# Performance work log

Measured on AMD Instinct MI355X. Metric: run time of the kernel, lower is better.

Reference implementation:

```python
import jax, jax.numpy as jnp
import numpy as np

K = 512
D = 256


def setup_inputs() -> dict:
    key = jax.random.key(0)
    k1, k2 = jax.random.split(key)
    x = jax.random.normal(k1, (64, D, 32, 32), dtype=jnp.float32)
    # nn.Embedding(K, D) init: uniform(-1/K, 1/K)
    emb = jax.random.uniform(k2, (K, D), dtype=jnp.float32, minval=-1.0 / K, maxval=1.0 / K)
    return {"x": x, "emb": emb}


def reference(x, emb):
    # encoder is identity: z_e_x = x, shape [B, D, H, W]
    B, Dd, H, W = x.shape
    z_e = jnp.transpose(x, (0, 2, 3, 1))           # [B, H, W, D]
    z_flat = z_e.reshape(-1, Dd)                    # [N, D]
    # squared euclidean distances to codebook: ||z||^2 + ||e||^2 - 2 z.e
    dist = (jnp.sum(z_flat * z_flat, axis=1, keepdims=True)
            + jnp.sum(emb * emb, axis=1)[None, :]
            - 2.0 * z_flat @ emb.T)                 # [N, K]
    idx = jnp.argmin(dist, axis=1)                  # [N]
    codes = emb[idx]                                # [N, D] gather
    codes = codes.reshape(B, H, W, Dd)
    # straight-through quantized output (value == codes)
    z_q_st = z_e + jax.lax.stop_gradient(codes - z_e)
    z_q_st = jnp.transpose(z_q_st, (0, 3, 1, 2))    # [B, D, H, W]
    # z_q_x_bar: gathered from live codebook (grads flow to emb)
    z_q_bar = jnp.transpose(codes, (0, 3, 1, 2))    # [B, D, H, W]
    # decoder is identity: x_tilde = z_q_st
    return (z_q_st, x, z_q_bar)
```

## Files before the change

### kernel.cpp

```cpp
#include <hip/hip_runtime.h>


#define B_  64
#define D_  256
#define HW_ 1024
#define K_  512

typedef __attribute__((ext_vector_type(8))) short short8;
typedef __attribute__((ext_vector_type(4))) float f32x4;

__device__ unsigned short g_ebf[K_ * D_];
__device__ float g_e2[K_];

__device__ __forceinline__ unsigned short f2bf(float f) {
    unsigned u = __float_as_uint(f);
    u += 0x7fffu + ((u >> 16) & 1u);
    return (unsigned short)(u >> 16);
}

__global__ void prep(const float* __restrict__ emb) {
    const int t   = threadIdx.x;
    const int row = blockIdx.x * 8 + (t >> 5);
    const int c0  = (t & 31) * 8;
    const float* rp = emb + row * D_ + c0;
    float4 a = *(const float4*)rp;
    float4 b = *(const float4*)(rp + 4);
    short8 v;
    v[0] = (short)f2bf(a.x); v[1] = (short)f2bf(a.y);
    v[2] = (short)f2bf(a.z); v[3] = (short)f2bf(a.w);
    v[4] = (short)f2bf(b.x); v[5] = (short)f2bf(b.y);
    v[6] = (short)f2bf(b.z); v[7] = (short)f2bf(b.w);
    *(short8*)(g_ebf + row * D_ + c0) = v;
    float ps = a.x*a.x + a.y*a.y + a.z*a.z + a.w*a.w
             + b.x*b.x + b.y*b.y + b.z*b.z + b.w*b.w;
    ps += __shfl_xor(ps, 1);  ps += __shfl_xor(ps, 2);
    ps += __shfl_xor(ps, 4);  ps += __shfl_xor(ps, 8);
    ps += __shfl_xor(ps, 16);
    if ((t & 31) == 0) g_e2[row] = ps;
}

__global__ __launch_bounds__(128, 4)
void vq_main(const float* __restrict__ x, const float* __restrict__ emb,
             float* __restrict__ out0, float* __restrict__ out1,
             float* __restrict__ out2) {
    __shared__ float zc[4][32][32];
    __shared__ float mval[2][32];
    __shared__ int   midx[2][32];
    __shared__ int   fidx[32];

    const int t   = threadIdx.x;
    const int w   = t >> 6;
    const int l   = t & 63;
    const int blk = blockIdx.x;
    const int b   = blk >> 5;
    const int hw0 = (blk & 31) << 5;
    const float* xb = x    + ((size_t)b * D_) * HW_ + hw0;
    float*       o1 = out1 + ((size_t)b * D_) * HW_ + hw0;

    short8 zb[2][8];
    for (int r = 0; r < 2; ++r) {
#pragma unroll
        for (int gg = 0; gg < 2; ++gg) {
            const int g = 4 * r + 2 * w + gg;
#pragma unroll
            for (int it = 0; it < 4; ++it) {
                const float* gp = xb + (size_t)(32 * g + 8 * it + (l >> 3)) * HW_ + (l & 7) * 4;
                float* lp = &zc[g & 3][8 * it][0];
                __builtin_amdgcn_global_load_lds(
                    (const __attribute__((address_space(1))) unsigned int*)gp,
                    (__attribute__((address_space(3))) unsigned int*)lp,
                    16, 0, 0);
            }
        }
        __syncthreads();
#pragma unroll
        for (int g4 = 0; g4 < 4; ++g4) {
            const int g = 4 * r + g4;
#pragma unroll
            for (int t2 = 0; t2 < 2; ++t2) {
                const int p = 16 * t2 + (l & 15);
                short8 f;
#pragma unroll
                for (int j = 0; j < 8; ++j)
                    f[j] = (short)f2bf(zc[g4][(l >> 4) * 8 + j][p]);
                zb[t2][g] = f;
            }
        }
#pragma unroll
        for (int gg = 0; gg < 2; ++gg) {
            const int g = 4 * r + 2 * w + gg;
#pragma unroll
            for (int it = 0; it < 4; ++it) {
                const int dr = 32 * g + 8 * it + (l >> 3);
                float4 v = *(const float4*)&zc[g & 3][8 * it + (l >> 3)][(l & 7) * 4];
                *(float4*)&o1[(size_t)dr * HW_ + (l & 7) * 4] = v;
            }
        }
        __syncthreads();
    }

    float minv0 = 3.0e38f, minv1 = 3.0e38f;
    int   mini0 = 0,       mini1 = 0;
    short8 ea[8], eb[8];
    f32x4  e2a, e2b;
    const int ctbase = w * 16;

#define LOADE(buf, e2r, ct) do {                                              \
        const unsigned short* _p = g_ebf + ((ct) * 16 + (l & 15)) * D_        \
                                   + (l >> 4) * 8;                            \
        _Pragma("unroll")                                                     \
        for (int s = 0; s < 8; ++s) buf[s] = *(const short8*)(_p + s * 32);   \
        e2r = *(const f32x4*)(g_e2 + (ct) * 16 + (l >> 4) * 4);               \
    } while (0)

#define PROC(buf, e2v, ct) do {                                               \
        f32x4 a0 = {0.f, 0.f, 0.f, 0.f}, a1 = {0.f, 0.f, 0.f, 0.f};          \
        _Pragma("unroll")                                                     \
        for (int s = 0; s < 8; ++s) {                                         \
            a0 = __builtin_amdgcn_mfma_f32_16x16x32_bf16(buf[s], zb[0][s], a0, 0, 0, 0); \
            a1 = __builtin_amdgcn_mfma_f32_16x16x32_bf16(buf[s], zb[1][s], a1, 0, 0, 0); \
        }                                                                     \
        _Pragma("unroll")                                                     \
        for (int r = 0; r < 4; ++r) {                                         \
            const int code = (ct) * 16 + (l >> 4) * 4 + r;                    \
            const float s0 = e2v[r] - 2.0f * a0[r];                           \
            const float s1 = e2v[r] - 2.0f * a1[r];                           \
            if (s0 < minv0) { minv0 = s0; mini0 = code; }                     \
            if (s1 < minv1) { minv1 = s1; mini1 = code; }                     \
        }                                                                     \
    } while (0)

    LOADE(ea, e2a, ctbase);
    for (int c = 0; c < 16; c += 2) {
        LOADE(eb, e2b, ctbase + c + 1);
        PROC(ea, e2a, ctbase + c);
        const int cn = (c + 2 < 16) ? (ctbase + c + 2) : ctbase;
        LOADE(ea, e2a, cn);
        PROC(eb, e2b, ctbase + c + 1);
    }

    {
        float ov; int oi;
        ov = __shfl_xor(minv0, 16); oi = __shfl_xor(mini0, 16);
        if (ov < minv0 || (ov == minv0 && oi < mini0)) { minv0 = ov; mini0 = oi; }
        ov = __shfl_xor(minv0, 32); oi = __shfl_xor(mini0, 32);
        if (ov < minv0 || (ov == minv0 && oi < mini0)) { minv0 = ov; mini0 = oi; }
        ov = __shfl_xor(minv1, 16); oi = __shfl_xor(mini1, 16);
        if (ov < minv1 || (ov == minv1 && oi < mini1)) { minv1 = ov; mini1 = oi; }
        ov = __shfl_xor(minv1, 32); oi = __shfl_xor(mini1, 32);
        if (ov < minv1 || (ov == minv1 && oi < mini1)) { minv1 = ov; mini1 = oi; }
    }
    if ((l >> 4) == 0) {
        mval[w][l & 15]      = minv0; midx[w][l & 15]      = mini0;
        mval[w][16 + (l & 15)] = minv1; midx[w][16 + (l & 15)] = mini1;
    }
    __syncthreads();
    if (t < 32) {
        const float v0 = mval[0][t], v1 = mval[1][t];
        fidx[t] = (v1 < v0) ? midx[1][t] : midx[0][t];
    }
    __syncthreads();

    {
        const int n  = t & 31;
        const int dg = t >> 5;
        const float* erow = emb + (size_t)fidx[n] * D_;
        float* p0 = out0 + ((size_t)b * D_) * HW_ + hw0 + n;
        float* p2 = out2 + ((size_t)b * D_) * HW_ + hw0 + n;
#pragma unroll 4
        for (int i = 0; i < 16; ++i) {
            const int d = dg * 4 + i * 16;
            float4 v = *(const float4*)&erow[d];
            p0[(size_t)(d + 0) * HW_] = v.x; p0[(size_t)(d + 1) * HW_] = v.y;
            p0[(size_t)(d + 2) * HW_] = v.z; p0[(size_t)(d + 3) * HW_] = v.w;
            p2[(size_t)(d + 0) * HW_] = v.x; p2[(size_t)(d + 1) * HW_] = v.y;
            p2[(size_t)(d + 2) * HW_] = v.z; p2[(size_t)(d + 3) * HW_] = v.w;
        }
    }
}

extern "C" void kernel_launch(void* const* d_in, const int* in_sizes, int n_in,
                              void* d_out, int out_size, void* d_ws, size_t ws_size,
                              hipStream_t stream) {
    const float* x   = (const float*)d_in[0];
    const float* emb = (const float*)d_in[1];
    float* out0 = (float*)d_out;
    float* out1 = out0 + (size_t)16777216;
    float* out2 = out0 + (size_t)33554432;

    prep<<<64, 256, 0, stream>>>(emb);
    vq_main<<<2048, 128, 0, stream>>>(x, emb, out0, out1, out2);
}
```

Baseline: 314.1 us.

## Split VQ into argmin and coalesced scatter kernels with transposed codebook

Separates the distance/argmin computation from output writing: the argmin kernel only stores indices to a global buffer, and a new scatter kernel writes all three outputs with coalesced float4 nontemporal stores, gathering code values from a transposed fp32 codebook built in prep. This replaces strided scalar column stores of codes with contiguous row stores. It costs an extra kernel launch, a second read of x, and an index round-trip through global memory.

```diff
diff --git a/kernel.cpp b/kernel.cpp
--- a/kernel.cpp
+++ b/kernel.cpp
@@ -11,6 +11,8 @@
 
 __device__ unsigned short g_ebf[K_ * D_];
 __device__ float g_e2[K_];
+__device__ float g_embT[D_ * K_];
+__device__ int   g_idx[B_ * HW_];
 
 __device__ __forceinline__ unsigned short f2bf(float f) {
     unsigned u = __float_as_uint(f);
@@ -31,6 +33,14 @@
     v[4] = (short)f2bf(b.x); v[5] = (short)f2bf(b.y);
     v[6] = (short)f2bf(b.z); v[7] = (short)f2bf(b.w);
     *(short8*)(g_ebf + row * D_ + c0) = v;
+    g_embT[(c0 + 0) * K_ + row] = a.x;
+    g_embT[(c0 + 1) * K_ + row] = a.y;
+    g_embT[(c0 + 2) * K_ + row] = a.z;
+    g_embT[(c0 + 3) * K_ + row] = a.w;
+    g_embT[(c0 + 4) * K_ + row] = b.x;
+    g_embT[(c0 + 5) * K_ + row] = b.y;
+    g_embT[(c0 + 6) * K_ + row] = b.z;
+    g_embT[(c0 + 7) * K_ + row] = b.w;
     float ps = a.x*a.x + a.y*a.y + a.z*a.z + a.w*a.w
              + b.x*b.x + b.y*b.y + b.z*b.z + b.w*b.w;
     ps += __shfl_xor(ps, 1);  ps += __shfl_xor(ps, 2);
@@ -40,13 +50,10 @@
 }
 
 __global__ __launch_bounds__(128, 4)
-void vq_main(const float* __restrict__ x, const float* __restrict__ emb,
-             float* __restrict__ out0, float* __restrict__ out1,
-             float* __restrict__ out2) {
+void vq_argmin(const float* __restrict__ x) {
     __shared__ float zc[4][32][32];
     __shared__ float mval[2][32];
     __shared__ int   midx[2][32];
-    __shared__ int   fidx[32];
 
     const int t   = threadIdx.x;
     const int w   = t >> 6;
@@ -54,8 +61,7 @@
     const int blk = blockIdx.x;
     const int b   = blk >> 5;
     const int hw0 = (blk & 31) << 5;
-    const float* xb = x    + ((size_t)b * D_) * HW_ + hw0;
-    float*       o1 = out1 + ((size_t)b * D_) * HW_ + hw0;
+    const float* xb = x + ((size_t)b * D_) * HW_ + hw0;
 
     short8 zb[2][8];
     for (int r = 0; r < 2; ++r) {
@@ -84,16 +90,6 @@
                 for (int j = 0; j < 8; ++j)
                     f[j] = (short)f2bf(zc[g4][(l >> 4) * 8 + j][p]);
                 zb[t2][g] = f;
-            }
-        }
-#pragma unroll
-        for (int gg = 0; gg < 2; ++gg) {
-            const int g = 4 * r + 2 * w + gg;
-#pragma unroll
-            for (int it = 0; it < 4; ++it) {
-                const int dr = 32 * g + 8 * it + (l >> 3);
-                float4 v = *(const float4*)&zc[g & 3][8 * it + (l >> 3)][(l & 7) * 4];
-                *(float4*)&o1[(size_t)dr * HW_ + (l & 7) * 4] = v;
             }
         }
         __syncthreads();
@@ -151,31 +147,40 @@
         if (ov < minv1 || (ov == minv1 && oi < mini1)) { minv1 = ov; mini1 = oi; }
     }
     if ((l >> 4) == 0) {
-        mval[w][l & 15]      = minv0; midx[w][l & 15]      = mini0;
+        mval[w][l & 15]        = minv0; midx[w][l & 15]        = mini0;
         mval[w][16 + (l & 15)] = minv1; midx[w][16 + (l & 15)] = mini1;
     }
     __syncthreads();
     if (t < 32) {
         const float v0 = mval[0][t], v1 = mval[1][t];
-        fidx[t] = (v1 < v0) ? midx[1][t] : midx[0][t];
+        g_idx[b * HW_ + hw0 + t] = (v1 < v0) ? midx[1][t] : midx[0][t];
     }
-    __syncthreads();
+}
 
-    {
-        const int n  = t & 31;
-        const int dg = t >> 5;
-        const float* erow = emb + (size_t)fidx[n] * D_;
-        float* p0 = out0 + ((size_t)b * D_) * HW_ + hw0 + n;
-        float* p2 = out2 + ((size_t)b * D_) * HW_ + hw0 + n;
+__global__ __launch_bounds__(256)
+void vq_scatter(const float* __restrict__ x, float* __restrict__ out0,
+                float* __restrict__ out1, float* __restrict__ out2) {
+    const int t   = threadIdx.x;
+    const int blk = blockIdx.x;
+    const int b   = blk >> 4;
+    const int d0  = (blk & 15) << 4;
+    const int4 mi = *(const int4*)(g_idx + b * HW_ + 4 * t);
+    const size_t base = ((size_t)b * D_ + d0) * HW_ + 4 * t;
+    const float* xp = x + base;
+    float* p0 = out0 + base;
+    float* p1 = out1 + base;
+    float* p2 = out2 + base;
 #pragma unroll 4
-        for (int i = 0; i < 16; ++i) {
-            const int d = dg * 4 + i * 16;
-            float4 v = *(const float4*)&erow[d];
-            p0[(size_t)(d + 0) * HW_] = v.x; p0[(size_t)(d + 1) * HW_] = v.y;
-            p0[(size_t)(d + 2) * HW_] = v.z; p0[(size_t)(d + 3) * HW_] = v.w;
-            p2[(size_t)(d + 0) * HW_] = v.x; p2[(size_t)(d + 1) * HW_] = v.y;
-            p2[(size_t)(d + 2) * HW_] = v.z; p2[(size_t)(d + 3) * HW_] = v.w;
-        }
+    for (int r = 0; r < 16; ++r) {
+        const float* et = g_embT + (size_t)(d0 + r) * K_;
+        const size_t off = (size_t)r * HW_;
+        f32x4 xv = *(const f32x4*)(xp + off);
+        f32x4 cv;
+        cv[0] = et[mi.x]; cv[1] = et[mi.y];
+        cv[2] = et[mi.z]; cv[3] = et[mi.w];
+        __builtin_nontemporal_store(xv, (f32x4*)(p1 + off));
+        __builtin_nontemporal_store(cv, (f32x4*)(p0 + off));
+        __builtin_nontemporal_store(cv, (f32x4*)(p2 + off));
     }
 }
 
@@ -189,5 +194,6 @@
     float* out2 = out0 + (size_t)33554432;
 
     prep<<<64, 256, 0, stream>>>(emb);
-    vq_main<<<2048, 128, 0, stream>>>(x, emb, out0, out1, out2);
+    vq_argmin<<<2048, 128, 0, stream>>>(x);
+    vq_scatter<<<1024, 256, 0, stream>>>(x, out0, out1, out2);
 }
```

Measured after the change: 319.1 us. Within noise of the previous version (+1.6%).
